# Kernel optimization log

Hardware: AMD Instinct MI355X
Metric: run time of the kernel (lower is better)

## Reference

```python
import jax, jax.numpy as jnp
import numpy as np

N = 1024        # total atoms
H = 256         # hidden_dim
L = 512         # latent_dim
NG = 50         # n_gaussians
NI = 3          # n_interactions
CUTOFF = 5.0
MAXZ = 100
B = 16          # molecules (N // 64 atoms each)

CENTERS = jnp.linspace(0.0, CUTOFF, NG)
WIDTH = 0.5 * (CUTOFF / NG)   # scalar, same for all gaussians
LN_EPS = 1e-5

def gelu(x):
    return jax.nn.gelu(x, approximate=False)  # torch default GELU is exact erf

def setup_inputs() -> dict:
    key = jax.random.key(0)
    ks = jax.random.split(key, 24)
    s = 0.05
    inp = {
        'z': jax.random.randint(ks[0], (N,), 0, MAXZ),
        'pos': jax.random.uniform(ks[1], (N, 3), dtype=jnp.float32) * 10.0,  # 10 A box
        'batch': jnp.arange(N, dtype=jnp.int32) // (N // B),
        'emb': jax.random.normal(ks[2], (MAXZ, H), dtype=jnp.float32),
        # per-interaction params stacked over layer axis (NI)
        'fw1': jax.random.normal(ks[3], (NI, NG, H), dtype=jnp.float32) * s,
        'fb1': jnp.zeros((NI, H), jnp.float32),
        'fw2': jax.random.normal(ks[4], (NI, H, H), dtype=jnp.float32) * s,
        'fb2': jnp.zeros((NI, H), jnp.float32),
        'aw1': jax.random.normal(ks[5], (NI, H, H), dtype=jnp.float32) * s,
        'ab1': jnp.zeros((NI, H), jnp.float32),
        'aw2': jax.random.normal(ks[6], (NI, H, H), dtype=jnp.float32) * s,
        'ab2': jnp.zeros((NI, H), jnp.float32),
        # projection head
        'pw1': jax.random.normal(ks[7], (H, H), dtype=jnp.float32) * s,
        'pb1': jnp.zeros((H,), jnp.float32),
        'pw2': jax.random.normal(ks[8], (H, L), dtype=jnp.float32) * s,
        'pb2': jnp.zeros((L,), jnp.float32),
        'ln_g': jnp.ones((L,), jnp.float32),
        'ln_b': jnp.zeros((L,), jnp.float32),
    }
    return inp

def _interaction(h, pos, fw1, fb1, fw2, fb2, aw1, ab1, aw2, ab2):
    diff = pos[None, :, :] - pos[:, None, :]              # [N,N,3]
    dist = jnp.linalg.norm(diff, axis=-1)                  # [N,N]
    mask = (dist < CUTOFF) & (dist > 1e-6)                 # [N,N]
    rbf = jnp.exp(-((dist[..., None] - CENTERS) ** 2) / (2.0 * WIDTH ** 2))  # [N,N,NG]
    W = gelu(rbf @ fw1 + fb1) @ fw2 + fb2                  # [N,N,H] filter MLP
    Wm = W * mask[..., None].astype(W.dtype)
    # agg[i,c] = sum_j Wm[i,j,c] * h[j,c]
    agg = jnp.einsum('ijc,jc->ic', Wm, h)
    return gelu(agg @ aw1 + ab1) @ aw2 + ab2

def reference(z, pos, batch, emb, fw1, fb1, fw2, fb2, aw1, ab1, aw2, ab2,
              pw1, pb1, pw2, pb2, ln_g, ln_b):
    h = emb[z]                                             # [N,H]
    for i in range(NI):
        h = h + _interaction(h, pos, fw1[i], fb1[i], fw2[i], fb2[i],
                             aw1[i], ab1[i], aw2[i], ab2[i])
    pooled = jax.ops.segment_sum(h, batch, num_segments=B)  # [B,H]
    x = gelu(pooled @ pw1 + pb1) @ pw2 + pb2               # [B,L]
    mu = jnp.mean(x, axis=-1, keepdims=True)
    var = jnp.var(x, axis=-1, keepdims=True)
    return (x - mu) / jnp.sqrt(var + LN_EPS) * ln_g + ln_b
```

## Files before the change

### kernel.cpp

```cpp
#include <hip/hip_runtime.h>
#include <hip/hip_fp16.h>
#include <math.h>

#define N 1024
#define H 256
#define L 512
#define NG 50
#define NI 3
#define B 16
#define NBINS 2048
#define CUT 5.0f
#define BPB 16
#define TROWS (NBINS + 1)
#define MATB 4
#define CAP 768
#define APAD 264

typedef __attribute__((ext_vector_type(8))) short bf16x8;
typedef __attribute__((ext_vector_type(4))) float f32x4;

#define FMA4(A_, S_, V_) do { \
    (A_).x = fmaf((S_), (V_).x, (A_).x); (A_).y = fmaf((S_), (V_).y, (A_).y); \
    (A_).z = fmaf((S_), (V_).z, (A_).z); (A_).w = fmaf((S_), (V_).w, (A_).w); } while (0)

__device__ __forceinline__ float gelu_f(float x) {
    return 0.5f * x * (1.0f + erff(x * 0.70710678118654752f));
}
__device__ __forceinline__ unsigned short f2bf(float f) {
    unsigned u = __float_as_uint(f);
    unsigned r = (u + 0x7fffu + ((u >> 16) & 1u)) >> 16;
    return (unsigned short)r;
}

__global__ void __launch_bounds__(256) setup_k(
        const int* __restrict__ z, const float* __restrict__ emb,
        const float* __restrict__ pos, float* __restrict__ h,
        __half* __restrict__ hhf, int* __restrict__ meta,
        int* __restrict__ cnts, const float* __restrict__ fw2,
        unsigned short* __restrict__ Bt, __half* __restrict__ Wtb) {
    int tid = threadIdx.x;
    if (blockIdx.x >= N) {
        int blk = blockIdx.x - N;
        int l = blk / H, ch = blk % H;
        float v = fw2[((size_t)l * H + tid) * H + ch];
        Bt[((size_t)l * H + ch) * H + tid] = f2bf(v);
        if (tid == 0)
            Wtb[((size_t)l * TROWS + NBINS) * H + ch] = __float2half(0.f);
        return;
    }
    int i = blockIdx.x;
    float v = emb[z[i] * H + tid];
    h[i * H + tid] = v;
    hhf[i * H + tid] = __float2half(v);

    __shared__ int sCnt;
    __shared__ int sMeta[CAP];
    if (tid == 0) sCnt = 0;
    __syncthreads();
    float pix = pos[i * 3 + 0], piy = pos[i * 3 + 1], piz = pos[i * 3 + 2];
    const float invd = (float)NBINS / CUT;
    for (int r = 0; r < 4; ++r) {
        int j = tid + r * 256;
        float dx = pos[j * 3 + 0] - pix;
        float dy = pos[j * 3 + 1] - piy;
        float dz = pos[j * 3 + 2] - piz;
        float d = sqrtf(dx * dx + dy * dy + dz * dz);
        if (d < CUT && d > 1e-6f) {
            int bin = (int)(d * invd);
            if (bin > NBINS - 1) bin = NBINS - 1;
            int idx = atomicAdd(&sCnt, 1);
            sMeta[idx] = j | (bin << 10);
        }
    }
    __syncthreads();
    int cnt = sCnt;
    int pc = (cnt + 31) & ~31;
    for (int t = cnt + tid; t < pc; t += 256)
        sMeta[t] = i | (NBINS << 10);
    __syncthreads();
    for (int t = tid; t < pc; t += 256)
        meta[(size_t)i * CAP + t] = sMeta[t];
    if (tid == 0) cnts[i] = pc;
}

__global__ void __launch_bounds__(256) table_k(
        const float* __restrict__ fw1, const float* __restrict__ fb1,
        const unsigned short* __restrict__ Bt, const float* __restrict__ fb2,
        __half* __restrict__ Wtb) {
    const int bpl = NBINS / BPB;
    int layer = blockIdx.x / bpl;
    int blk = blockIdx.x % bpl;
    int b0 = blk * BPB;
    int tid = threadIdx.x;
    int wid = tid >> 6, lane = tid & 63;
    int c4 = lane * 4;
    int ub = wid * 4;
    const float* lfw1 = fw1 + layer * NG * H;
    __half* lWt = Wtb + (size_t)layer * TROWS * H;

    __shared__ __align__(16) float sW1[NG][H];
    __shared__ __align__(16) float sRbf[BPB][56];
    __shared__ __align__(16) unsigned short sAb[BPB][APAD];
    const float delta = CUT / (float)NBINS;
    for (int idx = tid; idx < NG * (H / 4); idx += 256) {
        int k = idx >> 6;
        int c = (idx & 63) * 4;
        *(float4*)&sW1[k][c] = *(const float4*)(lfw1 + k * H + c);
    }
    for (int idx = tid; idx < BPB * NG; idx += 256) {
        int u = idx & 15;
        int k = idx >> 4;
        float d = ((float)(b0 + u) + 0.5f) * delta;
        float t = d - (float)k * (CUT / 49.0f);
        sRbf[u][k] = expf(t * t * -200.0f);
    }
    __syncthreads();

    float4 acc1[4];
    #pragma unroll
    for (int u = 0; u < 4; ++u) acc1[u] = make_float4(0.f, 0.f, 0.f, 0.f);
    for (int kq = 0; kq < 12; ++kq) {
        int k = kq * 4;
        float4 r0 = *(const float4*)&sRbf[ub + 0][k];
        float4 r1 = *(const float4*)&sRbf[ub + 1][k];
        float4 r2 = *(const float4*)&sRbf[ub + 2][k];
        float4 r3 = *(const float4*)&sRbf[ub + 3][k];
        float4 q0 = *(const float4*)&sW1[k + 0][c4];
        float4 q1 = *(const float4*)&sW1[k + 1][c4];
        float4 q2 = *(const float4*)&sW1[k + 2][c4];
        float4 q3 = *(const float4*)&sW1[k + 3][c4];
        FMA4(acc1[0], r0.x, q0); FMA4(acc1[0], r0.y, q1);
        FMA4(acc1[0], r0.z, q2); FMA4(acc1[0], r0.w, q3);
        FMA4(acc1[1], r1.x, q0); FMA4(acc1[1], r1.y, q1);
        FMA4(acc1[1], r1.z, q2); FMA4(acc1[1], r1.w, q3);
        FMA4(acc1[2], r2.x, q0); FMA4(acc1[2], r2.y, q1);
        FMA4(acc1[2], r2.z, q2); FMA4(acc1[2], r2.w, q3);
        FMA4(acc1[3], r3.x, q0); FMA4(acc1[3], r3.y, q1);
        FMA4(acc1[3], r3.z, q2); FMA4(acc1[3], r3.w, q3);
    }
    for (int k = 48; k < NG; ++k) {
        float4 q = *(const float4*)&sW1[k][c4];
        #pragma unroll
        for (int u = 0; u < 4; ++u) FMA4(acc1[u], sRbf[ub + u][k], q);
    }
    float4 b1 = *(const float4*)(fb1 + layer * H + c4);
    #pragma unroll
    for (int u = 0; u < 4; ++u) {
        ushort4 g;
        g.x = f2bf(gelu_f(acc1[u].x + b1.x));
        g.y = f2bf(gelu_f(acc1[u].y + b1.y));
        g.z = f2bf(gelu_f(acc1[u].z + b1.z));
        g.w = f2bf(gelu_f(acc1[u].w + b1.w));
        *(ushort4*)&sAb[ub + u][c4] = g;
    }
    __syncthreads();

    int m = lane & 15;
    int quad = lane >> 4;
    bf16x8 afr[8];
    #pragma unroll
    for (int c = 0; c < 8; ++c)
        afr[c] = *(const bf16x8*)&sAb[m][c * 32 + quad * 8];
    #pragma unroll
    for (int ct = 0; ct < 4; ++ct) {
        int chn = (wid * 4 + ct) * 16 + m;
        const bf16x8* Bv = (const bf16x8*)(Bt + ((size_t)layer * H + chn) * H);
        f32x4 acc = {0.f, 0.f, 0.f, 0.f};
        #pragma unroll
        for (int c = 0; c < 8; ++c)
            acc = __builtin_amdgcn_mfma_f32_16x16x32_bf16(afr[c], Bv[c * 4 + quad],
                                                          acc, 0, 0, 0);
        float bias = fb2[layer * H + chn];
        #pragma unroll
        for (int r = 0; r < 4; ++r) {
            int bin = b0 + quad * 4 + r;
            lWt[(size_t)bin * H + chn] = __float2half(acc[r] + bias);
        }
    }
}

__global__ void __launch_bounds__(256) pair_k(
    const __half* __restrict__ hhf, const __half* __restrict__ Wt,
    const int* __restrict__ gmeta, const int* __restrict__ cnts,
    float* __restrict__ aggP) {
    int tid = threadIdx.x;
    int wid = tid >> 6, lane = tid & 63;
    int c4 = lane * 4;
    int i = blockIdx.x >> 1;
    int half = blockIdx.x & 1;
    int stream = half * 4 + wid;

    __shared__ int sMeta[CAP];
    __shared__ __align__(16) float sPart[4][H];

    int pc = cnts[i];
    for (int t = tid; t < pc; t += 256)
        sMeta[t] = gmeta[(size_t)i * CAP + t];
    __syncthreads();

    float4 acc = make_float4(0.f, 0.f, 0.f, 0.f);
    int groups = pc >> 5;

    uint2 wA[4], wB[4];
    uint2 hA[4], hB[4];

    auto issue = [&](int g, uint2 (&wr)[4], uint2 (&hr)[4]) {
        #pragma unroll
        for (int s = 0; s < 4; ++s) {
            int n = stream + (g * 4 + s) * 8;
            int p = sMeta[n];
            int j = p & 1023;
            int bin = p >> 10;
            wr[s] = *(const uint2*)(Wt + (size_t)bin * H + c4);
            hr[s] = *(const uint2*)(hhf + (size_t)j * H + c4);
        }
    };
    auto consume = [&](uint2 (&wr)[4], uint2 (&hr)[4]) {
        #pragma unroll
        for (int s = 0; s < 4; ++s) {
            __half2 w01 = *(__half2*)&wr[s].x;
            __half2 w23 = *(__half2*)&wr[s].y;
            __half2 h01 = *(__half2*)&hr[s].x;
            __half2 h23 = *(__half2*)&hr[s].y;
            acc.x += __half2float(w01.x) * __half2float(h01.x);
            acc.y += __half2float(w01.y) * __half2float(h01.y);
            acc.z += __half2float(w23.x) * __half2float(h23.x);
            acc.w += __half2float(w23.y) * __half2float(h23.y);
        }
    };

    if (groups > 0) {
        issue(0, wA, hA);
        if (groups > 1) issue(1, wB, hB);
        for (int g = 0; g < groups; g += 2) {
            consume(wA, hA);
            if (g + 2 < groups) issue(g + 2, wA, hA);
            if (g + 1 < groups) {
                consume(wB, hB);
                if (g + 3 < groups) issue(g + 3, wB, hB);
            }
        }
    }
    *(float4*)&sPart[wid][c4] = acc;
    __syncthreads();
    aggP[((size_t)half * N + i) * H + tid] =
        sPart[0][tid] + sPart[1][tid] + sPart[2][tid] + sPart[3][tid];
}

__global__ void __launch_bounds__(512) mlp_k(
    const float* __restrict__ aggP, const float* __restrict__ hin,
    const float* __restrict__ aw1, const float* __restrict__ ab1,
    const float* __restrict__ aw2, const float* __restrict__ ab2,
    float* __restrict__ hout, __half* __restrict__ hhf_out) {
    int tid = threadIdx.x;
    int wid = tid >> 6, lane = tid & 63;
    int c4 = lane * 4;
    int i0 = blockIdx.x * MATB;
    __shared__ __align__(16) float sAT[H][MATB];
    __shared__ __align__(16) float sGT[H][MATB];
    __shared__ __align__(16) float sPart[8][MATB][H];

    if (tid < H) {
        #pragma unroll
        for (int r = 0; r < MATB; ++r)
            sAT[tid][r] = aggP[(size_t)(i0 + r) * H + tid]
                        + aggP[((size_t)N + i0 + r) * H + tid];
    }
    __syncthreads();

    int k0 = wid * 32;
    float4 acc[MATB];
    #pragma unroll
    for (int a = 0; a < MATB; ++a) acc[a] = make_float4(0.f, 0.f, 0.f, 0.f);
    #pragma unroll 8
    for (int k = 0; k < 32; ++k) {
        float4 q = *(const float4*)(aw1 + (k0 + k) * H + c4);
        float4 act = *(const float4*)&sAT[k0 + k][0];
        FMA4(acc[0], act.x, q); FMA4(acc[1], act.y, q);
        FMA4(acc[2], act.z, q); FMA4(acc[3], act.w, q);
    }
    #pragma unroll
    for (int a = 0; a < MATB; ++a)
        *(float4*)&sPart[wid][a][c4] = acc[a];
    __syncthreads();
    if (tid < H) {
        float b1 = ab1[tid];
        float g[MATB];
        #pragma unroll
        for (int a = 0; a < MATB; ++a) {
            float v = b1;
            #pragma unroll
            for (int s = 0; s < 8; ++s) v += sPart[s][a][tid];
            g[a] = gelu_f(v);
        }
        *(float4*)&sGT[tid][0] = make_float4(g[0], g[1], g[2], g[3]);
    }
    __syncthreads();
    #pragma unroll
    for (int a = 0; a < MATB; ++a) acc[a] = make_float4(0.f, 0.f, 0.f, 0.f);
    #pragma unroll 8
    for (int k = 0; k < 32; ++k) {
        float4 q = *(const float4*)(aw2 + (k0 + k) * H + c4);
        float4 act = *(const float4*)&sGT[k0 + k][0];
        FMA4(acc[0], act.x, q); FMA4(acc[1], act.y, q);
        FMA4(acc[2], act.z, q); FMA4(acc[3], act.w, q);
    }
    #pragma unroll
    for (int a = 0; a < MATB; ++a)
        *(float4*)&sPart[wid][a][c4] = acc[a];
    __syncthreads();
    if (tid < H) {
        float b2 = ab2[tid];
        #pragma unroll
        for (int a = 0; a < MATB; ++a) {
            float v = b2;
            #pragma unroll
            for (int s = 0; s < 8; ++s) v += sPart[s][a][tid];
            float hv = hin[(i0 + a) * H + tid] + v;
            hout[(i0 + a) * H + tid] = hv;
            hhf_out[(i0 + a) * H + tid] = __float2half(hv);
        }
    }
}

__global__ void __launch_bounds__(256) head_k(
        const float* __restrict__ h,
        const float* __restrict__ pw1, const float* __restrict__ pb1,
        const float* __restrict__ pw2, const float* __restrict__ pb2,
        const float* __restrict__ ln_g, const float* __restrict__ ln_b,
        float* __restrict__ out) {
    int b = blockIdx.x, tid = threadIdx.x;
    int wid = tid >> 6, lane = tid & 63;
    int c4 = lane * 4;
    __shared__ float sP[H];
    __shared__ __align__(16) float sPw[4][H];
    __shared__ float sG[H];
    __shared__ __align__(16) float sP2[4][L];
    __shared__ float sX[L];
    __shared__ float sRed[256];

    float4 p = make_float4(0.f, 0.f, 0.f, 0.f);
    #pragma unroll 4
    for (int a = 0; a < 16; ++a) {
        float4 hv = *(const float4*)(h + (b * 64 + wid * 16 + a) * H + c4);
        p.x += hv.x; p.y += hv.y; p.z += hv.z; p.w += hv.w;
    }
    *(float4*)&sPw[wid][c4] = p;
    __syncthreads();
    sP[tid] = sPw[0][tid] + sPw[1][tid] + sPw[2][tid] + sPw[3][tid];
    __syncthreads();

    int k0 = wid * 64;
    float4 acc = make_float4(0.f, 0.f, 0.f, 0.f);
    #pragma unroll 8
    for (int k = 0; k < 64; ++k) {
        float4 q = *(const float4*)(pw1 + (k0 + k) * H + c4);
        float s = sP[k0 + k];
        FMA4(acc, s, q);
    }
    *(float4*)&sPw[wid][c4] = acc;
    __syncthreads();
    sG[tid] = gelu_f(pb1[tid] + sPw[0][tid] + sPw[1][tid] + sPw[2][tid] + sPw[3][tid]);
    __syncthreads();

    float4 a0 = make_float4(0.f, 0.f, 0.f, 0.f);
    float4 a1 = make_float4(0.f, 0.f, 0.f, 0.f);
    #pragma unroll 4
    for (int k = 0; k < 64; ++k) {
        float s = sG[k0 + k];
        float4 q0 = *(const float4*)(pw2 + (k0 + k) * L + lane * 8);
        float4 q1 = *(const float4*)(pw2 + (k0 + k) * L + lane * 8 + 4);
        FMA4(a0, s, q0);
        FMA4(a1, s, q1);
    }
    *(float4*)&sP2[wid][lane * 8] = a0;
    *(float4*)&sP2[wid][lane * 8 + 4] = a1;
    __syncthreads();
    for (int r = 0; r < 2; ++r) {
        int l = tid + r * 256;
        sX[l] = pb2[l] + sP2[0][l] + sP2[1][l] + sP2[2][l] + sP2[3][l];
    }
    __syncthreads();

    sRed[tid] = sX[tid] + sX[tid + 256];
    __syncthreads();
    for (int off = 128; off > 0; off >>= 1) {
        if (tid < off) sRed[tid] += sRed[tid + off];
        __syncthreads();
    }
    float mu = sRed[0] / (float)L;
    __syncthreads();
    float d0 = sX[tid] - mu, d1 = sX[tid + 256] - mu;
    sRed[tid] = d0 * d0 + d1 * d1;
    __syncthreads();
    for (int off = 128; off > 0; off >>= 1) {
        if (tid < off) sRed[tid] += sRed[tid + off];
        __syncthreads();
    }
    float var = sRed[0] / (float)L;
    float rstd = rsqrtf(var + 1e-5f);
    for (int r = 0; r < 2; ++r) {
        int l = tid + r * 256;
        out[b * L + l] = (sX[l] - mu) * rstd * ln_g[l] + ln_b[l];
    }
}

extern "C" void kernel_launch(void* const* d_in, const int* in_sizes, int n_in,
                              void* d_out, int out_size, void* d_ws, size_t ws_size,
                              hipStream_t stream) {
    const int*   z    = (const int*)d_in[0];
    const float* pos  = (const float*)d_in[1];
    const float* emb  = (const float*)d_in[3];
    const float* fw1  = (const float*)d_in[4];
    const float* fb1  = (const float*)d_in[5];
    const float* fw2  = (const float*)d_in[6];
    const float* fb2  = (const float*)d_in[7];
    const float* aw1  = (const float*)d_in[8];
    const float* ab1  = (const float*)d_in[9];
    const float* aw2  = (const float*)d_in[10];
    const float* ab2  = (const float*)d_in[11];
    const float* pw1  = (const float*)d_in[12];
    const float* pb1  = (const float*)d_in[13];
    const float* pw2  = (const float*)d_in[14];
    const float* pb2  = (const float*)d_in[15];
    const float* ln_g = (const float*)d_in[16];
    const float* ln_b = (const float*)d_in[17];
    float* out = (float*)d_out;

    float* hA  = (float*)d_ws;
    float* hB  = hA + N * H;
    float* aggP = hB + N * H;
    __half* hhfA = (__half*)(aggP + 2 * N * H);
    __half* hhfB = hhfA + N * H;
    __half* Wtb  = hhfB + N * H;
    int* meta = (int*)(Wtb + (size_t)NI * TROWS * H);
    int* cnts = meta + (size_t)N * CAP;
    unsigned short* Bt = (unsigned short*)(cnts + N);

    setup_k<<<N + NI * H, 256, 0, stream>>>(z, emb, pos, hA, hhfA, meta, cnts,
                                            fw2, Bt, Wtb);
    table_k<<<NI * (NBINS / BPB), 256, 0, stream>>>(fw1, fb1, Bt, fb2, Wtb);
    float* hin = hA;  __half* hbin = hhfA;
    float* hout = hB; __half* hbout = hhfB;
    for (int it = 0; it < NI; ++it) {
        pair_k<<<2 * N, 256, 0, stream>>>(hbin, Wtb + (size_t)it * TROWS * H,
                                          meta, cnts, aggP);
        mlp_k<<<N / MATB, 512, 0, stream>>>(aggP, hin, aw1 + it * H * H, ab1 + it * H,
                                            aw2 + it * H * H, ab2 + it * H, hout, hbout);
        float* t1 = hin; hin = hout; hout = t1;
        __half* t2 = hbin; hbin = hbout; hbout = t2;
    }
    head_k<<<B, 256, 0, stream>>>(hin, pw1, pb1, pw2, pb2, ln_g, ln_b, out);
}
```

Before: 236.8 us.

## Run per-atom interaction MLP on bf16 MFMA with pre-transposed weights

Replaces the fp32 FMA-based atom MLP (4 atoms per block, 512 threads) with a bf16 MFMA 16x16x32 version that handles 16 atoms per block using 256 threads. The setup kernel gains extra blocks that transpose aw1/aw2 into bf16 so each MFMA lane can read contiguous weight fragments. This cuts the number of MLP blocks and the repeated weight reads, in exchange for bf16 rounding of the activations and weights. It also adds more setup blocks.

```diff
diff --git a/kernel.cpp b/kernel.cpp
--- a/kernel.cpp
+++ b/kernel.cpp
@@ -12,7 +12,6 @@
 #define CUT 5.0f
 #define BPB 16
 #define TROWS (NBINS + 1)
-#define MATB 4
 #define CAP 768
 #define APAD 264
 
@@ -37,15 +36,29 @@
         const float* __restrict__ pos, float* __restrict__ h,
         __half* __restrict__ hhf, int* __restrict__ meta,
         int* __restrict__ cnts, const float* __restrict__ fw2,
-        unsigned short* __restrict__ Bt, __half* __restrict__ Wtb) {
+        unsigned short* __restrict__ Bt, __half* __restrict__ Wtb,
+        const float* __restrict__ aw1, const float* __restrict__ aw2,
+        unsigned short* __restrict__ awT1, unsigned short* __restrict__ awT2) {
     int tid = threadIdx.x;
     if (blockIdx.x >= N) {
         int blk = blockIdx.x - N;
-        int l = blk / H, ch = blk % H;
-        float v = fw2[((size_t)l * H + tid) * H + ch];
-        Bt[((size_t)l * H + ch) * H + tid] = f2bf(v);
-        if (tid == 0)
-            Wtb[((size_t)l * TROWS + NBINS) * H + ch] = __float2half(0.f);
+        if (blk < NI * H) {
+            int l = blk / H, ch = blk % H;
+            float v = fw2[((size_t)l * H + tid) * H + ch];
+            Bt[((size_t)l * H + ch) * H + tid] = f2bf(v);
+            if (tid == 0)
+                Wtb[((size_t)l * TROWS + NBINS) * H + ch] = __float2half(0.f);
+        } else if (blk < 2 * NI * H) {
+            int b2 = blk - NI * H;
+            int l = b2 / H, n = b2 % H;
+            awT1[((size_t)l * H + n) * H + tid] =
+                f2bf(aw1[((size_t)l * H + tid) * H + n]);
+        } else {
+            int b2 = blk - 2 * NI * H;
+            int l = b2 / H, n = b2 % H;
+            awT2[((size_t)l * H + n) * H + tid] =
+                f2bf(aw2[((size_t)l * H + tid) * H + n]);
+        }
         return;
     }
     int i = blockIdx.x;
@@ -247,78 +260,66 @@
         sPart[0][tid] + sPart[1][tid] + sPart[2][tid] + sPart[3][tid];
 }
 
-__global__ void __launch_bounds__(512) mlp_k(
+__global__ void __launch_bounds__(256) mlp_k(
     const float* __restrict__ aggP, const float* __restrict__ hin,
-    const float* __restrict__ aw1, const float* __restrict__ ab1,
-    const float* __restrict__ aw2, const float* __restrict__ ab2,
+    const unsigned short* __restrict__ awT1, const float* __restrict__ ab1,
+    const unsigned short* __restrict__ awT2, const float* __restrict__ ab2,
     float* __restrict__ hout, __half* __restrict__ hhf_out) {
     int tid = threadIdx.x;
     int wid = tid >> 6, lane = tid & 63;
-    int c4 = lane * 4;
-    int i0 = blockIdx.x * MATB;
-    __shared__ __align__(16) float sAT[H][MATB];
-    __shared__ __align__(16) float sGT[H][MATB];
-    __shared__ __align__(16) float sPart[8][MATB][H];
-
-    if (tid < H) {
-        #pragma unroll
-        for (int r = 0; r < MATB; ++r)
-            sAT[tid][r] = aggP[(size_t)(i0 + r) * H + tid]
-                        + aggP[((size_t)N + i0 + r) * H + tid];
-    }
-    __syncthreads();
-
-    int k0 = wid * 32;
-    float4 acc[MATB];
-    #pragma unroll
-    for (int a = 0; a < MATB; ++a) acc[a] = make_float4(0.f, 0.f, 0.f, 0.f);
-    #pragma unroll 8
-    for (int k = 0; k < 32; ++k) {
-        float4 q = *(const float4*)(aw1 + (k0 + k) * H + c4);
-        float4 act = *(const float4*)&sAT[k0 + k][0];
-        FMA4(acc[0], act.x, q); FMA4(acc[1], act.y, q);
-        FMA4(acc[2], act.z, q); FMA4(acc[3], act.w, q);
-    }
-    #pragma unroll
-    for (int a = 0; a < MATB; ++a)
-        *(float4*)&sPart[wid][a][c4] = acc[a];
-    __syncthreads();
-    if (tid < H) {
-        float b1 = ab1[tid];
-        float g[MATB];
-        #pragma unroll
-        for (int a = 0; a < MATB; ++a) {
-            float v = b1;
-            #pragma unroll
-            for (int s = 0; s < 8; ++s) v += sPart[s][a][tid];
-            g[a] = gelu_f(v);
-        }
-        *(float4*)&sGT[tid][0] = make_float4(g[0], g[1], g[2], g[3]);
-    }
-    __syncthreads();
-    #pragma unroll
-    for (int a = 0; a < MATB; ++a) acc[a] = make_float4(0.f, 0.f, 0.f, 0.f);
-    #pragma unroll 8
-    for (int k = 0; k < 32; ++k) {
-        float4 q = *(const float4*)(aw2 + (k0 + k) * H + c4);
-        float4 act = *(const float4*)&sGT[k0 + k][0];
-        FMA4(acc[0], act.x, q); FMA4(acc[1], act.y, q);
-        FMA4(acc[2], act.z, q); FMA4(acc[3], act.w, q);
-    }
-    #pragma unroll
-    for (int a = 0; a < MATB; ++a)
-        *(float4*)&sPart[wid][a][c4] = acc[a];
-    __syncthreads();
-    if (tid < H) {
-        float b2 = ab2[tid];
-        #pragma unroll
-        for (int a = 0; a < MATB; ++a) {
-            float v = b2;
-            #pragma unroll
-            for (int s = 0; s < 8; ++s) v += sPart[s][a][tid];
-            float hv = hin[(i0 + a) * H + tid] + v;
-            hout[(i0 + a) * H + tid] = hv;
-            hhf_out[(i0 + a) * H + tid] = __float2half(hv);
+    int m = lane & 15, quad = lane >> 4;
+    int i0 = blockIdx.x * 16;
+    __shared__ __align__(16) unsigned short sA[16][APAD];
+    __shared__ __align__(16) unsigned short sG[16][APAD];
+
+    for (int e = tid; e < 16 * H; e += 256) {
+        int a = e >> 8, c = e & 255;
+        float v = aggP[(size_t)(i0 + a) * H + c]
+                + aggP[((size_t)N + i0 + a) * H + c];
+        sA[a][c] = f2bf(v);
+    }
+    __syncthreads();
+
+    bf16x8 afr[8];
+    #pragma unroll
+    for (int c = 0; c < 8; ++c)
+        afr[c] = *(const bf16x8*)&sA[m][c * 32 + quad * 8];
+    #pragma unroll
+    for (int nt = 0; nt < 4; ++nt) {
+        int n = (wid * 4 + nt) * 16 + m;
+        const bf16x8* Bv = (const bf16x8*)(awT1 + (size_t)n * H);
+        f32x4 acc = {0.f, 0.f, 0.f, 0.f};
+        #pragma unroll
+        for (int c = 0; c < 8; ++c)
+            acc = __builtin_amdgcn_mfma_f32_16x16x32_bf16(afr[c], Bv[c * 4 + quad],
+                                                          acc, 0, 0, 0);
+        float b1 = ab1[n];
+        #pragma unroll
+        for (int r = 0; r < 4; ++r)
+            sG[quad * 4 + r][n] = f2bf(gelu_f(acc[r] + b1));
+    }
+    __syncthreads();
+
+    bf16x8 gfr[8];
+    #pragma unroll
+    for (int c = 0; c < 8; ++c)
+        gfr[c] = *(const bf16x8*)&sG[m][c * 32 + quad * 8];
+    #pragma unroll
+    for (int nt = 0; nt < 4; ++nt) {
+        int n = (wid * 4 + nt) * 16 + m;
+        const bf16x8* Bv = (const bf16x8*)(awT2 + (size_t)n * H);
+        f32x4 acc = {0.f, 0.f, 0.f, 0.f};
+        #pragma unroll
+        for (int c = 0; c < 8; ++c)
+            acc = __builtin_amdgcn_mfma_f32_16x16x32_bf16(gfr[c], Bv[c * 4 + quad],
+                                                          acc, 0, 0, 0);
+        float b2 = ab2[n];
+        #pragma unroll
+        for (int r = 0; r < 4; ++r) {
+            int atom = i0 + quad * 4 + r;
+            float hv = hin[(size_t)atom * H + n] + acc[r] + b2;
+            hout[(size_t)atom * H + n] = hv;
+            hhf_out[(size_t)atom * H + n] = __float2half(hv);
         }
     }
 }
@@ -436,17 +437,21 @@
     int* meta = (int*)(Wtb + (size_t)NI * TROWS * H);
     int* cnts = meta + (size_t)N * CAP;
     unsigned short* Bt = (unsigned short*)(cnts + N);
-
-    setup_k<<<N + NI * H, 256, 0, stream>>>(z, emb, pos, hA, hhfA, meta, cnts,
-                                            fw2, Bt, Wtb);
+    unsigned short* awT1 = Bt + (size_t)NI * H * H;
+    unsigned short* awT2 = awT1 + (size_t)NI * H * H;
+
+    setup_k<<<N + 3 * NI * H, 256, 0, stream>>>(z, emb, pos, hA, hhfA, meta, cnts,
+                                                fw2, Bt, Wtb, aw1, aw2, awT1, awT2);
     table_k<<<NI * (NBINS / BPB), 256, 0, stream>>>(fw1, fb1, Bt, fb2, Wtb);
     float* hin = hA;  __half* hbin = hhfA;
     float* hout = hB; __half* hbout = hhfB;
     for (int it = 0; it < NI; ++it) {
         pair_k<<<2 * N, 256, 0, stream>>>(hbin, Wtb + (size_t)it * TROWS * H,
                                           meta, cnts, aggP);
-        mlp_k<<<N / MATB, 512, 0, stream>>>(aggP, hin, aw1 + it * H * H, ab1 + it * H,
-                                            aw2 + it * H * H, ab2 + it * H, hout, hbout);
+        mlp_k<<<N / 16, 256, 0, stream>>>(aggP, hin,
+                                          awT1 + (size_t)it * H * H, ab1 + it * H,
+                                          awT2 + (size_t)it * H * H, ab2 + it * H,
+                                          hout, hbout);
         float* t1 = hin; hin = hout; hout = t1;
         __half* t2 = hbin; hbin = hbout; hbout = t2;
     }
```

Measured after the change: 250.2 us. +5.6%, slower.
